# Kernel optimization log

Measured on AMD Instinct MI355X. Metric: run time of the kernel, lower is better.

## Reference

```python
import jax, jax.numpy as jnp
import numpy as np

N = 50000      # nodes (single 'paper' node type)
E = 800000     # edges per etype
ET = 3         # edge types
L = 3          # GAT layers (1 + num_hidden=2)
H = 4          # heads
DH = 64        # per-head dim (n_hidden // n_heads)
NH = H * DH    # 256
NC = 16        # classes
NEG_SLOPE = 0.2


def setup_inputs() -> dict:
    key = jax.random.key(0)
    ks = jax.random.split(key, 8)
    x = jax.random.normal(ks[0], (N, NH), jnp.float32)
    src = jax.random.randint(ks[1], (ET, E), 0, N, jnp.int32)
    dst = jax.random.randint(ks[2], (ET, E), 0, N, jnp.int32)
    W = jax.random.normal(ks[3], (L, ET, NH, NH), jnp.float32) * 0.05
    attn_l = jax.random.normal(ks[4], (L, ET, H, DH), jnp.float32) * 0.05
    attn_r = jax.random.normal(ks[5], (L, ET, H, DH), jnp.float32) * 0.05
    bias = jnp.zeros((L, ET, NH), jnp.float32)
    lin_w = jax.random.normal(ks[6], (NH, NC), jnp.float32) * 0.05
    lin_b = jnp.zeros((NC,), jnp.float32)
    return {"x": x, "src": src, "dst": dst, "W": W, "attn_l": attn_l,
            "attn_r": attn_r, "bias": bias, "lin_w": lin_w, "lin_b": lin_b}


def _gat(h, W_e, al, ar, b, s, d):
    # h: [N, NH] -> z: [N, H, DH]
    z = (h @ W_e).reshape(N, H, DH)
    el = jnp.sum(z * al, axis=-1)             # [N, H]  (src-side score)
    er = jnp.sum(z * ar, axis=-1)             # [N, H]  (dst-side score)
    e = jax.nn.leaky_relu(el[s] + er[d], NEG_SLOPE)   # [E, H]
    # edge softmax over incoming edges of each dst node
    m = jax.ops.segment_max(e, d, num_segments=N)     # [N, H]
    a = jnp.exp(e - m[d])                              # [E, H]
    denom = jax.ops.segment_sum(a, d, num_segments=N) # [N, H]
    alpha = a / denom[d]                               # [E, H]
    # weighted aggregation of source features
    out = jax.ops.segment_sum(alpha[:, :, None] * z[s], d, num_segments=N)  # [N, H, DH]
    return out.reshape(N, NH) + b


def reference(x, src, dst, W, attn_l, attn_r, bias, lin_w, lin_b):
    h = x
    for l in range(L):
        acc = jnp.zeros((N, NH), h.dtype)
        for t in range(ET):  # HeteroGraphConv 'sum' aggregation across etypes
            acc = acc + _gat(h, W[l, t], attn_l[l, t], attn_r[l, t],
                             bias[l, t], src[t], dst[t])
        h = acc
        if l != L - 1:
            h = jax.nn.relu(h)  # dropout is identity in eval
    return h @ lin_w + lin_b    # [N, NC]
```

## Files before the change

kernel.cpp:

```cpp
#include <hip/hip_runtime.h>
#include <hip/hip_bf16.h>
#include <math.h>

#define N_NODES 50000
#define NEDGE 800000
#define NET 3
#define LAYERS 3
#define HEADS 4
#define DHEAD 64
#define NH 256
#define NC 16
#define NEG_SLOPE 0.2f
#define MPAD 50048
#define NTOT (NET * N_NODES)
#define SCAN_BLOCKS ((NTOT + 1023) / 1024)

typedef __attribute__((ext_vector_type(8))) short short8;
typedef __attribute__((ext_vector_type(4))) float f32x4;
typedef __attribute__((ext_vector_type(8))) _Float16 half8;

#define GLDS16(gp, lp) \
  __builtin_amdgcn_global_load_lds((const __attribute__((address_space(1))) void*)(gp), \
                                   (__attribute__((address_space(3))) void*)(lp), 16, 0, 0)

__device__ inline unsigned short f2bf(float x) {
  unsigned u = __float_as_uint(x);
  unsigned r = (u + 0x7FFFu + ((u >> 16) & 1u)) >> 16;
  return (unsigned short)r;
}
__device__ inline float bf2f(unsigned short h) { return __uint_as_float(((unsigned)h) << 16); }

__global__ void split_transpose_W(const float* __restrict__ W,
                                  unsigned short* __restrict__ WhT,
                                  unsigned short* __restrict__ WlT) {
  int i = blockIdx.x * blockDim.x + threadIdx.x;
  if (i >= LAYERS * NET * NH * NH) return;
  int mat = i >> 16, rem = i & 65535;
  int n = rem >> 8, k = rem & 255;
  float v = W[(size_t)mat * 65536 + k * 256 + n];
  unsigned short hi = f2bf(v);
  unsigned short lo = f2bf(v - bf2f(hi));
  WhT[(size_t)mat * 65536 + n * 256 + k] = hi;
  WlT[(size_t)mat * 65536 + n * 256 + k] = lo;
}

__global__ void split_kernel(const float* __restrict__ in, unsigned short* __restrict__ hi,
                             unsigned short* __restrict__ lo) {
  int i = blockIdx.x * blockDim.x + threadIdx.x;
  if (i >= N_NODES * NH / 4) return;
  float4 v = ((const float4*)in)[i];
  ushort4 h, l;
  h.x = f2bf(v.x); l.x = f2bf(v.x - bf2f(h.x));
  h.y = f2bf(v.y); l.y = f2bf(v.y - bf2f(h.y));
  h.z = f2bf(v.z); l.z = f2bf(v.z - bf2f(h.z));
  h.w = f2bf(v.w); l.w = f2bf(v.w - bf2f(h.w));
  ((ushort4*)hi)[i] = h;
  ((ushort4*)lo)[i] = l;
}

__global__ __launch_bounds__(256) void gemm_split3(const unsigned short* __restrict__ Ah,
                                                   const unsigned short* __restrict__ Al,
                                                   const unsigned short* __restrict__ WhT_l,
                                                   const unsigned short* __restrict__ WlT_l,
                                                   const float* __restrict__ attn_l_l,
                                                   const float* __restrict__ attn_r_l,
                                                   _Float16* __restrict__ zh_all,
                                                   float* __restrict__ el_all,
                                                   float* __restrict__ er_all, int M) {
  int t = blockIdx.y;
  const unsigned short* BhT = WhT_l + (size_t)t * NH * NH;
  const unsigned short* BlT = WlT_l + (size_t)t * NH * NH;
  const float* al = attn_l_l + (size_t)t * NH;
  const float* ar = attn_r_l + (size_t)t * NH;
  _Float16* zh = zh_all + (size_t)t * N_NODES * NH;
  float* el = el_all + (size_t)t * N_NODES * HEADS;
  float* er = er_all + (size_t)t * N_NODES * HEADS;

  __shared__ unsigned short lds[20480];
  unsigned short* sAh = lds;
  unsigned short* sAl = lds + 2048;
  unsigned short* sBh = lds + 4096;
  unsigned short* sBl = lds + 12288;

  int tid = threadIdx.x;
  int w = tid >> 6, lane = tid & 63;
  int r16 = lane & 15, rk = lane >> 4;
  int bm = blockIdx.x * 64;

  int arow = tid >> 2, acol = (tid & 3) * 8;
  const unsigned short* pAh = Ah + (size_t)(bm + arow) * 256 + acol;
  const unsigned short* pAl = Al + (size_t)(bm + arow) * 256 + acol;

  f32x4 acc[4][4];
#pragma unroll
  for (int m = 0; m < 4; m++)
#pragma unroll
    for (int n = 0; n < 4; n++) acc[m][n] = (f32x4){0.f, 0.f, 0.f, 0.f};

  char* aldsA = (char*)lds + (size_t)w * 1024;

#pragma unroll
  for (int k0 = 0; k0 < 8; k0++) {
    GLDS16(pAh + k0 * 32, aldsA);
    GLDS16(pAl + k0 * 32, (char*)sAl + (size_t)w * 1024);
#pragma unroll
    for (int i = 0; i < 4; i++) {
      int slot = tid + i * 256;
      int nrow = slot >> 2, kcol = (slot & 3) * 8;
      size_t go = (size_t)nrow * 256 + k0 * 32 + kcol;
      char* lb = (char*)sBh + ((size_t)w * 64 + (size_t)i * 256) * 16;
      char* lb2 = (char*)sBl + ((size_t)w * 64 + (size_t)i * 256) * 16;
      GLDS16(BhT + go, lb);
      GLDS16(BlT + go, lb2);
    }
    __syncthreads();

    short8 a_h[4], a_l[4], b_h[4], b_l[4];
#pragma unroll
    for (int m = 0; m < 4; m++) {
      a_h[m] = *(const short8*)&sAh[(m * 16 + r16) * 32 + rk * 8];
      a_l[m] = *(const short8*)&sAl[(m * 16 + r16) * 32 + rk * 8];
    }
#pragma unroll
    for (int n = 0; n < 4; n++) {
      int col = w * 64 + n * 16 + r16;
      b_h[n] = *(const short8*)&sBh[col * 32 + rk * 8];
      b_l[n] = *(const short8*)&sBl[col * 32 + rk * 8];
    }
#pragma unroll
    for (int m = 0; m < 4; m++)
#pragma unroll
      for (int n = 0; n < 4; n++) {
        acc[m][n] = __builtin_amdgcn_mfma_f32_16x16x32_bf16(a_h[m], b_h[n], acc[m][n], 0, 0, 0);
        acc[m][n] = __builtin_amdgcn_mfma_f32_16x16x32_bf16(a_h[m], b_l[n], acc[m][n], 0, 0, 0);
        acc[m][n] = __builtin_amdgcn_mfma_f32_16x16x32_bf16(a_l[m], b_h[n], acc[m][n], 0, 0, 0);
      }
    __syncthreads();
  }

#pragma unroll
  for (int m = 0; m < 4; m++) {
    int row0 = bm + m * 16 + rk * 4;
#pragma unroll
    for (int n = 0; n < 4; n++) {
      int col = w * 64 + n * 16 + r16;
#pragma unroll
      for (int r = 0; r < 4; r++) {
        int row = row0 + r;
        if (row < M) zh[(size_t)row * 256 + col] = (_Float16)acc[m][n][r];
      }
    }
  }

  float alv[4], arv[4];
#pragma unroll
  for (int n = 0; n < 4; n++) {
    alv[n] = al[w * 64 + n * 16 + r16];
    arv[n] = ar[w * 64 + n * 16 + r16];
  }
#pragma unroll
  for (int m = 0; m < 4; m++) {
#pragma unroll
    for (int r = 0; r < 4; r++) {
      float pl = 0.f, pr = 0.f;
#pragma unroll
      for (int n = 0; n < 4; n++) {
        float zv = acc[m][n][r];
        pl = fmaf(zv, alv[n], pl);
        pr = fmaf(zv, arv[n], pr);
      }
      pl += __shfl_xor(pl, 1, 64); pl += __shfl_xor(pl, 2, 64);
      pl += __shfl_xor(pl, 4, 64); pl += __shfl_xor(pl, 8, 64);
      pr += __shfl_xor(pr, 1, 64); pr += __shfl_xor(pr, 2, 64);
      pr += __shfl_xor(pr, 4, 64); pr += __shfl_xor(pr, 8, 64);
      int row = bm + m * 16 + rk * 4 + r;
      if (r16 == 0 && row < M) {
        el[row * HEADS + w] = pl;
        er[row * HEADS + w] = pr;
      }
    }
  }
}

__device__ inline float leaky(float v) { return v > 0.f ? v : NEG_SLOPE * v; }

__global__ void deg_kernel(const int* __restrict__ dst, int* __restrict__ deg) {
  int e = blockIdx.x * blockDim.x + threadIdx.x;
  int t = blockIdx.y;
  atomicAdd(&deg[t * N_NODES + dst[(size_t)t * NEDGE + e]], 1);
}

__global__ __launch_bounds__(1024) void scan1_kernel(const int* __restrict__ deg,
                                                     int* __restrict__ incl,
                                                     int* __restrict__ bsum) {
  __shared__ int wsum[16];
  int tid = threadIdx.x;
  int gid = blockIdx.x * 1024 + tid;
  int lane = tid & 63, wv = tid >> 6;
  int v = (gid < NTOT) ? deg[gid] : 0;
  int x = v;
#pragma unroll
  for (int off = 1; off < 64; off <<= 1) {
    int y = __shfl_up(x, off, 64);
    if (lane >= off) x += y;
  }
  if (lane == 63) wsum[wv] = x;
  __syncthreads();
  if (wv == 0 && lane < 16) {
    int s = wsum[lane];
#pragma unroll
    for (int off = 1; off < 16; off <<= 1) {
      int y = __shfl_up(s, off, 16);
      if (lane >= off) s += y;
    }
    wsum[lane] = s;
  }
  __syncthreads();
  int waveoff = (wv > 0) ? wsum[wv - 1] : 0;
  int inclv = x + waveoff;
  if (gid < NTOT) incl[gid] = inclv;
  if (tid == 1023) bsum[blockIdx.x] = inclv;
}

__global__ __launch_bounds__(256) void scan2_kernel(int* __restrict__ bsum, int nb) {
  __shared__ int wsum[4];
  int tid = threadIdx.x;
  int lane = tid & 63, wv = tid >> 6;
  int v = (tid < nb) ? bsum[tid] : 0;
  int x = v;
#pragma unroll
  for (int off = 1; off < 64; off <<= 1) {
    int y = __shfl_up(x, off, 64);
    if (lane >= off) x += y;
  }
  if (lane == 63) wsum[wv] = x;
  __syncthreads();
  if (wv == 0 && lane < 4) {
    int s = wsum[lane];
#pragma unroll
    for (int off = 1; off < 4; off <<= 1) {
      int y = __shfl_up(s, off, 4);
      if (lane >= off) s += y;
    }
    wsum[lane] = s;
  }
  __syncthreads();
  int waveoff = (wv > 0) ? wsum[wv - 1] : 0;
  if (tid < nb) bsum[tid] = x + waveoff - v;
}

__global__ __launch_bounds__(1024) void scan3_kernel(const int* __restrict__ incl,
                                                     const int* __restrict__ bsum,
                                                     int* __restrict__ rowptr) {
  int tid = threadIdx.x;
  int gid = blockIdx.x * 1024 + tid;
  if (gid < NTOT) rowptr[gid + 1] = incl[gid] + bsum[blockIdx.x];
  if (gid == 0) rowptr[0] = 0;
}

__global__ void scatter_kernel(const int* __restrict__ src, const int* __restrict__ dst,
                               int* __restrict__ cursor, int* __restrict__ col) {
  int e = blockIdx.x * blockDim.x + threadIdx.x;
  int t = blockIdx.y;
  int d = dst[(size_t)t * NEDGE + e];
  int pos = atomicAdd(&cursor[t * N_NODES + d], 1);
  col[pos] = src[(size_t)t * NEDGE + e] + t * N_NODES;
}

__global__ __launch_bounds__(256) void agg3_kernel(const int* __restrict__ rowptr,
                                                   const int* __restrict__ col,
                                                   const float* __restrict__ el,
                                                   const float* __restrict__ er,
                                                   const _Float16* __restrict__ zh,
                                                   float* __restrict__ hout,
                                                   unsigned short* __restrict__ Ah,
                                                   unsigned short* __restrict__ Al,
                                                   const float* __restrict__ b0,
                                                   const float* __restrict__ b1,
                                                   const float* __restrict__ b2,
                                                   int final_layer) {
  __shared__ float s_alpha[4][128][4];
  __shared__ int s_col[4][128];

  int wv = threadIdx.x >> 6, lane = threadIdx.x & 63;
  int n = blockIdx.x * 4 + wv;
  int kk = lane & 15, hh = lane >> 4;
  int which = lane >> 5, lj = lane & 31, fh = lj >> 3;

  float v0 = 0.f, v1 = 0.f, v2 = 0.f, v3 = 0.f;
  float v4 = 0.f, v5 = 0.f, v6 = 0.f, v7 = 0.f;

  for (int t = 0; t < NET; t++) {
    int gn = t * N_NODES + n;
    int rs = rowptr[gn];
    int deg = rowptr[gn + 1] - rs;
    float erh = er[(size_t)gn * HEADS + hh];

    float sm = 0.f;
    float a0 = 0.f, a1 = 0.f, a2 = 0.f, a3 = 0.f;
    float a4 = 0.f, a5 = 0.f, a6 = 0.f, a7 = 0.f;

    for (int s0 = 0; s0 < deg; s0 += 128) {
      int segN = min(128, deg - s0);
      for (int c0 = 0; c0 < segN; c0 += 16) {
        if (c0 + kk < segN) {
          int row = col[rs + s0 + c0 + kk];
          float a = __expf(leaky(el[(size_t)row * HEADS + hh] + erh));
          sm += a;
          s_alpha[wv][c0 + kk][hh] = a;
          if (hh == 0) s_col[wv][c0 + kk] = row;
        }
      }
      int k = which;
      for (; k + 6 < segN; k += 8) {
        float aa = s_alpha[wv][k][fh];     int ra = s_col[wv][k];
        float ab = s_alpha[wv][k + 2][fh]; int rb = s_col[wv][k + 2];
        float ac = s_alpha[wv][k + 4][fh]; int rc = s_col[wv][k + 4];
        float ad = s_alpha[wv][k + 6][fh]; int rd = s_col[wv][k + 6];
        half8 va = *(const half8*)&zh[(size_t)ra * NH + lj * 8];
        half8 vb = *(const half8*)&zh[(size_t)rb * NH + lj * 8];
        half8 vc = *(const half8*)&zh[(size_t)rc * NH + lj * 8];
        half8 vd = *(const half8*)&zh[(size_t)rd * NH + lj * 8];
        a0 = fmaf(aa, (float)va[0], a0); a1 = fmaf(aa, (float)va[1], a1);
        a2 = fmaf(aa, (float)va[2], a2); a3 = fmaf(aa, (float)va[3], a3);
        a4 = fmaf(aa, (float)va[4], a4); a5 = fmaf(aa, (float)va[5], a5);
        a6 = fmaf(aa, (float)va[6], a6); a7 = fmaf(aa, (float)va[7], a7);
        a0 = fmaf(ab, (float)vb[0], a0); a1 = fmaf(ab, (float)vb[1], a1);
        a2 = fmaf(ab, (float)vb[2], a2); a3 = fmaf(ab, (float)vb[3], a3);
        a4 = fmaf(ab, (float)vb[4], a4); a5 = fmaf(ab, (float)vb[5], a5);
        a6 = fmaf(ab, (float)vb[6], a6); a7 = fmaf(ab, (float)vb[7], a7);
        a0 = fmaf(ac, (float)vc[0], a0); a1 = fmaf(ac, (float)vc[1], a1);
        a2 = fmaf(ac, (float)vc[2], a2); a3 = fmaf(ac, (float)vc[3], a3);
        a4 = fmaf(ac, (float)vc[4], a4); a5 = fmaf(ac, (float)vc[5], a5);
        a6 = fmaf(ac, (float)vc[6], a6); a7 = fmaf(ac, (float)vc[7], a7);
        a0 = fmaf(ad, (float)vd[0], a0); a1 = fmaf(ad, (float)vd[1], a1);
        a2 = fmaf(ad, (float)vd[2], a2); a3 = fmaf(ad, (float)vd[3], a3);
        a4 = fmaf(ad, (float)vd[4], a4); a5 = fmaf(ad, (float)vd[5], a5);
        a6 = fmaf(ad, (float)vd[6], a6); a7 = fmaf(ad, (float)vd[7], a7);
      }
      for (; k < segN; k += 2) {
        float aa = s_alpha[wv][k][fh];
        int ra = s_col[wv][k];
        half8 va = *(const half8*)&zh[(size_t)ra * NH + lj * 8];
        a0 = fmaf(aa, (float)va[0], a0); a1 = fmaf(aa, (float)va[1], a1);
        a2 = fmaf(aa, (float)va[2], a2); a3 = fmaf(aa, (float)va[3], a3);
        a4 = fmaf(aa, (float)va[4], a4); a5 = fmaf(aa, (float)va[5], a5);
        a6 = fmaf(aa, (float)va[6], a6); a7 = fmaf(aa, (float)va[7], a7);
      }
    }

    sm += __shfl_xor(sm, 1, 64);
    sm += __shfl_xor(sm, 2, 64);
    sm += __shfl_xor(sm, 4, 64);
    sm += __shfl_xor(sm, 8, 64);
    float inv = (deg > 0) ? 1.f / sm : 0.f;
    float invb = __shfl(inv, fh * 16, 64);

    a0 += __shfl_xor(a0, 32, 64); a1 += __shfl_xor(a1, 32, 64);
    a2 += __shfl_xor(a2, 32, 64); a3 += __shfl_xor(a3, 32, 64);
    a4 += __shfl_xor(a4, 32, 64); a5 += __shfl_xor(a5, 32, 64);
    a6 += __shfl_xor(a6, 32, 64); a7 += __shfl_xor(a7, 32, 64);

    v0 = fmaf(a0, invb, v0); v1 = fmaf(a1, invb, v1);
    v2 = fmaf(a2, invb, v2); v3 = fmaf(a3, invb, v3);
    v4 = fmaf(a4, invb, v4); v5 = fmaf(a5, invb, v5);
    v6 = fmaf(a6, invb, v6); v7 = fmaf(a7, invb, v7);
  }

  if (lane < 32) {
    int f0 = lj * 8;
    float vo[8] = {v0, v1, v2, v3, v4, v5, v6, v7};
#pragma unroll
    for (int i = 0; i < 8; i++) vo[i] += b0[f0 + i] + b1[f0 + i] + b2[f0 + i];
    if (final_layer) {
      size_t oi = (size_t)n * NH + f0;
      float4 o0 = {vo[0], vo[1], vo[2], vo[3]};
      float4 o1 = {vo[4], vo[5], vo[6], vo[7]};
      *(float4*)&hout[oi] = o0;
      *(float4*)&hout[oi + 4] = o1;
    } else {
      ushort4 hi0, hi1, lo0, lo1;
#pragma unroll
      for (int i = 0; i < 8; i++) vo[i] = fmaxf(vo[i], 0.f);
      hi0.x = f2bf(vo[0]); lo0.x = f2bf(vo[0] - bf2f(hi0.x));
      hi0.y = f2bf(vo[1]); lo0.y = f2bf(vo[1] - bf2f(hi0.y));
      hi0.z = f2bf(vo[2]); lo0.z = f2bf(vo[2] - bf2f(hi0.z));
      hi0.w = f2bf(vo[3]); lo0.w = f2bf(vo[3] - bf2f(hi0.w));
      hi1.x = f2bf(vo[4]); lo1.x = f2bf(vo[4] - bf2f(hi1.x));
      hi1.y = f2bf(vo[5]); lo1.y = f2bf(vo[5] - bf2f(hi1.y));
      hi1.z = f2bf(vo[6]); lo1.z = f2bf(vo[6] - bf2f(hi1.z));
      hi1.w = f2bf(vo[7]); lo1.w = f2bf(vo[7] - bf2f(hi1.w));
      size_t oi = (size_t)n * NH + f0;
      *(ushort4*)&Ah[oi] = hi0;
      *(ushort4*)&Ah[oi + 4] = hi1;
      *(ushort4*)&Al[oi] = lo0;
      *(ushort4*)&Al[oi + 4] = lo1;
    }
  }
}

__global__ __launch_bounds__(256) void linear_kernel(const float* __restrict__ h,
                                                     const float* __restrict__ w,
                                                     const float* __restrict__ b,
                                                     float* __restrict__ out) {
  __shared__ float part[16][17];
  int n = blockIdx.x;
  int t = threadIdx.x;
  int c = t & 15, p = t >> 4;
  float sum = 0.f;
#pragma unroll
  for (int q = 0; q < 16; q++) {
    int j = p * 16 + q;
    sum = fmaf(h[(size_t)n * NH + j], w[j * NC + c], sum);
  }
  part[p][c] = sum;
  __syncthreads();
  if (t < 16) {
    float s = 0.f;
#pragma unroll
    for (int p2 = 0; p2 < 16; p2++) s += part[p2][t];
    out[n * NC + t] = s + b[t];
  }
}

extern "C" void kernel_launch(void* const* d_in, const int* in_sizes, int n_in,
                              void* d_out, int out_size, void* d_ws, size_t ws_size,
                              hipStream_t stream) {
  const float* x      = (const float*)d_in[0];
  const int*   src    = (const int*)d_in[1];
  const int*   dst    = (const int*)d_in[2];
  const float* W      = (const float*)d_in[3];
  const float* attn_l = (const float*)d_in[4];
  const float* attn_r = (const float*)d_in[5];
  const float* bias   = (const float*)d_in[6];
  const float* lin_w  = (const float*)d_in[7];
  const float* lin_b  = (const float*)d_in[8];
  float* out = (float*)d_out;

  char* ws = (char*)d_ws;
  size_t off = 0;
  _Float16* zh = (_Float16*)(ws + off); off += (size_t)NET * N_NODES * NH * 2;
  unsigned short* Ah = (unsigned short*)(ws + off); off += (size_t)MPAD * NH * 2;
  unsigned short* Al = (unsigned short*)(ws + off); off += (size_t)MPAD * NH * 2;
  float* h = (float*)Ah;
  unsigned short* WhT = (unsigned short*)(ws + off); off += (size_t)LAYERS * NET * NH * NH * 2;
  unsigned short* WlT = (unsigned short*)(ws + off); off += (size_t)LAYERS * NET * NH * NH * 2;
  float* el = (float*)(ws + off); off += (size_t)NTOT * HEADS * 4;
  float* er = (float*)(ws + off); off += (size_t)NTOT * HEADS * 4;
  int* rowptr = (int*)(ws + off); off += (size_t)(NTOT + 1) * 4;
  int* colA   = (int*)(ws + off); off += (size_t)NET * NEDGE * 4;
  int* deg    = (int*)(ws + off); off += (size_t)NTOT * 4;
  int* cursor = (int*)(ws + off); off += (size_t)NTOT * 4;
  int* incl   = (int*)(ws + off); off += (size_t)NTOT * 4;
  int* bsum   = (int*)(ws + off); off += 256 * 4;

  hipMemsetAsync(deg, 0, (size_t)NTOT * 4, stream);
  deg_kernel<<<dim3(NEDGE / 256, NET), 256, 0, stream>>>(dst, deg);
  scan1_kernel<<<SCAN_BLOCKS, 1024, 0, stream>>>(deg, incl, bsum);
  scan2_kernel<<<1, 256, 0, stream>>>(bsum, SCAN_BLOCKS);
  scan3_kernel<<<SCAN_BLOCKS, 1024, 0, stream>>>(incl, bsum, rowptr);
  hipMemcpyAsync(cursor, rowptr, (size_t)NTOT * 4, hipMemcpyDeviceToDevice, stream);
  scatter_kernel<<<dim3(NEDGE / 256, NET), 256, 0, stream>>>(src, dst, cursor, colA);

  split_transpose_W<<<(LAYERS * NET * NH * NH + 255) / 256, 256, 0, stream>>>(W, WhT, WlT);

  split_kernel<<<(N_NODES * NH / 4 + 255) / 256, 256, 0, stream>>>(x, Ah, Al);

  for (int l = 0; l < LAYERS; l++) {
    const float* b0 = bias + (size_t)(l * NET + 0) * NH;
    const float* b1 = bias + (size_t)(l * NET + 1) * NH;
    const float* b2 = bias + (size_t)(l * NET + 2) * NH;

    gemm_split3<<<dim3(MPAD / 64, NET), 256, 0, stream>>>(
        Ah, Al,
        WhT + (size_t)l * NET * NH * NH, WlT + (size_t)l * NET * NH * NH,
        attn_l + (size_t)l * NET * NH, attn_r + (size_t)l * NET * NH,
        zh, el, er, N_NODES);

    agg3_kernel<<<N_NODES / 4, 256, 0, stream>>>(rowptr, colA, el, er, zh, h, Ah, Al,
                                                 b0, b1, b2, l == LAYERS - 1);
  }
  linear_kernel<<<N_NODES, 256, 0, stream>>>(h, lin_w, lin_b, out);
}
```

Measured before the change: 1.315 ms.

## Fuse prep kernels, overlap edge scatter with first GEMM, enlarge GEMM tile

Merges degree counting, feature split and weight split/transpose into one prep launch. Runs the CSR scatter and the layer-0 GEMM in a single launch using disjoint block ranges so the two overlap. Changes the GEMM to 512-thread blocks covering 128 rows, which halves the B-tile loads per output row. Also cuts the aggregation gather unroll from 4 to 2 neighbours per iteration, which may lower register pressure but exposes less memory parallelism.

```diff
diff --git a/kernel.cpp b/kernel.cpp
--- a/kernel.cpp
+++ b/kernel.cpp
@@ -14,6 +14,10 @@
 #define MPAD 50048
 #define NTOT (NET * N_NODES)
 #define SCAN_BLOCKS ((NTOT + 1023) / 1024)
+#define GB_PER_T 391
+#define GEMM_BLOCKS (GB_PER_T * NET)
+#define SCAT_PER_T 1563
+#define SCAT_BLOCKS (SCAT_PER_T * NET)
 
 typedef __attribute__((ext_vector_type(8))) short short8;
 typedef __attribute__((ext_vector_type(4))) float f32x4;
@@ -29,45 +33,60 @@
   return (unsigned short)r;
 }
 __device__ inline float bf2f(unsigned short h) { return __uint_as_float(((unsigned)h) << 16); }
-
-__global__ void split_transpose_W(const float* __restrict__ W,
-                                  unsigned short* __restrict__ WhT,
-                                  unsigned short* __restrict__ WlT) {
-  int i = blockIdx.x * blockDim.x + threadIdx.x;
-  if (i >= LAYERS * NET * NH * NH) return;
-  int mat = i >> 16, rem = i & 65535;
-  int n = rem >> 8, k = rem & 255;
-  float v = W[(size_t)mat * 65536 + k * 256 + n];
-  unsigned short hi = f2bf(v);
-  unsigned short lo = f2bf(v - bf2f(hi));
-  WhT[(size_t)mat * 65536 + n * 256 + k] = hi;
-  WlT[(size_t)mat * 65536 + n * 256 + k] = lo;
-}
-
-__global__ void split_kernel(const float* __restrict__ in, unsigned short* __restrict__ hi,
-                             unsigned short* __restrict__ lo) {
-  int i = blockIdx.x * blockDim.x + threadIdx.x;
-  if (i >= N_NODES * NH / 4) return;
-  float4 v = ((const float4*)in)[i];
-  ushort4 h, l;
-  h.x = f2bf(v.x); l.x = f2bf(v.x - bf2f(h.x));
-  h.y = f2bf(v.y); l.y = f2bf(v.y - bf2f(h.y));
-  h.z = f2bf(v.z); l.z = f2bf(v.z - bf2f(h.z));
-  h.w = f2bf(v.w); l.w = f2bf(v.w - bf2f(h.w));
-  ((ushort4*)hi)[i] = h;
-  ((ushort4*)lo)[i] = l;
-}
-
-__global__ __launch_bounds__(256) void gemm_split3(const unsigned short* __restrict__ Ah,
-                                                   const unsigned short* __restrict__ Al,
-                                                   const unsigned short* __restrict__ WhT_l,
-                                                   const unsigned short* __restrict__ WlT_l,
-                                                   const float* __restrict__ attn_l_l,
-                                                   const float* __restrict__ attn_r_l,
-                                                   _Float16* __restrict__ zh_all,
-                                                   float* __restrict__ el_all,
-                                                   float* __restrict__ er_all, int M) {
-  int t = blockIdx.y;
+__device__ inline float leaky(float v) { return v > 0.f ? v : NEG_SLOPE * v; }
+
+__global__ __launch_bounds__(256) void prep_kernel(const int* __restrict__ dst,
+                                                   int* __restrict__ deg,
+                                                   const float* __restrict__ x,
+                                                   unsigned short* __restrict__ Ah,
+                                                   unsigned short* __restrict__ Al,
+                                                   const float* __restrict__ W,
+                                                   unsigned short* __restrict__ WhT,
+                                                   unsigned short* __restrict__ WlT) {
+  int b = blockIdx.x;
+  if (b < 9375) {
+    int t = b / 3125, r = b % 3125;
+    int e = r * 256 + threadIdx.x;
+    atomicAdd(&deg[t * N_NODES + dst[(size_t)t * NEDGE + e]], 1);
+  } else if (b < 21875) {
+    int i = (b - 9375) * 256 + threadIdx.x;
+    float4 v = ((const float4*)x)[i];
+    ushort4 h, l;
+    h.x = f2bf(v.x); l.x = f2bf(v.x - bf2f(h.x));
+    h.y = f2bf(v.y); l.y = f2bf(v.y - bf2f(h.y));
+    h.z = f2bf(v.z); l.z = f2bf(v.z - bf2f(h.z));
+    h.w = f2bf(v.w); l.w = f2bf(v.w - bf2f(h.w));
+    ((ushort4*)Ah)[i] = h;
+    ((ushort4*)Al)[i] = l;
+  } else {
+    int i = (b - 21875) * 256 + threadIdx.x;
+    int mat = i >> 16, rem = i & 65535;
+    int n = rem >> 8, k = rem & 255;
+    float v = W[(size_t)mat * 65536 + k * 256 + n];
+    unsigned short hi = f2bf(v);
+    unsigned short lo = f2bf(v - bf2f(hi));
+    WhT[(size_t)mat * 65536 + n * 256 + k] = hi;
+    WlT[(size_t)mat * 65536 + n * 256 + k] = lo;
+  }
+}
+
+__device__ __forceinline__ void gemm_dev(int bid,
+                                         const unsigned short* __restrict__ Ah,
+                                         const unsigned short* __restrict__ Al,
+                                         const unsigned short* __restrict__ WhT_l,
+                                         const unsigned short* __restrict__ WlT_l,
+                                         const float* __restrict__ attn_l_l,
+                                         const float* __restrict__ attn_r_l,
+                                         _Float16* __restrict__ zh_all,
+                                         float* __restrict__ el_all,
+                                         float* __restrict__ er_all, int M) {
+  __shared__ unsigned short lds[24576];
+  unsigned short* sAh = lds;
+  unsigned short* sAl = lds + 4096;
+  unsigned short* sBh = lds + 8192;
+  unsigned short* sBl = lds + 16384;
+
+  int t = bid / GB_PER_T, bx = bid % GB_PER_T;
   const unsigned short* BhT = WhT_l + (size_t)t * NH * NH;
   const unsigned short* BlT = WlT_l + (size_t)t * NH * NH;
   const float* al = attn_l_l + (size_t)t * NH;
@@ -76,20 +95,14 @@
   float* el = el_all + (size_t)t * N_NODES * HEADS;
   float* er = er_all + (size_t)t * N_NODES * HEADS;
 
-  __shared__ unsigned short lds[20480];
-  unsigned short* sAh = lds;
-  unsigned short* sAl = lds + 2048;
-  unsigned short* sBh = lds + 4096;
-  unsigned short* sBl = lds + 12288;
-
   int tid = threadIdx.x;
   int w = tid >> 6, lane = tid & 63;
+  int rg = w >> 2, hd = w & 3;
   int r16 = lane & 15, rk = lane >> 4;
-  int bm = blockIdx.x * 64;
-
-  int arow = tid >> 2, acol = (tid & 3) * 8;
-  const unsigned short* pAh = Ah + (size_t)(bm + arow) * 256 + acol;
-  const unsigned short* pAl = Al + (size_t)(bm + arow) * 256 + acol;
+  int bm = bx * 128;
+
+  const unsigned short* pAh = Ah + (size_t)(bm + (tid >> 2)) * 256 + (tid & 3) * 8;
+  const unsigned short* pAl = Al + (size_t)(bm + (tid >> 2)) * 256 + (tid & 3) * 8;
 
   f32x4 acc[4][4];
 #pragma unroll
@@ -97,33 +110,32 @@
 #pragma unroll
     for (int n = 0; n < 4; n++) acc[m][n] = (f32x4){0.f, 0.f, 0.f, 0.f};
 
-  char* aldsA = (char*)lds + (size_t)w * 1024;
+  char* aBaseH = (char*)sAh + w * 1024;
+  char* aBaseL = (char*)sAl + w * 1024;
 
 #pragma unroll
   for (int k0 = 0; k0 < 8; k0++) {
-    GLDS16(pAh + k0 * 32, aldsA);
-    GLDS16(pAl + k0 * 32, (char*)sAl + (size_t)w * 1024);
-#pragma unroll
-    for (int i = 0; i < 4; i++) {
-      int slot = tid + i * 256;
-      int nrow = slot >> 2, kcol = (slot & 3) * 8;
-      size_t go = (size_t)nrow * 256 + k0 * 32 + kcol;
-      char* lb = (char*)sBh + ((size_t)w * 64 + (size_t)i * 256) * 16;
-      char* lb2 = (char*)sBl + ((size_t)w * 64 + (size_t)i * 256) * 16;
-      GLDS16(BhT + go, lb);
-      GLDS16(BlT + go, lb2);
+    GLDS16(pAh + k0 * 32, aBaseH);
+    GLDS16(pAl + k0 * 32, aBaseL);
+#pragma unroll
+    for (int i = 0; i < 2; i++) {
+      int slot = tid + i * 512;
+      size_t go = (size_t)(slot >> 2) * 256 + k0 * 32 + (slot & 3) * 8;
+      GLDS16(BhT + go, (char*)sBh + ((size_t)i * 512 + w * 64) * 16);
+      GLDS16(BlT + go, (char*)sBl + ((size_t)i * 512 + w * 64) * 16);
     }
     __syncthreads();
 
     short8 a_h[4], a_l[4], b_h[4], b_l[4];
 #pragma unroll
     for (int m = 0; m < 4; m++) {
-      a_h[m] = *(const short8*)&sAh[(m * 16 + r16) * 32 + rk * 8];
-      a_l[m] = *(const short8*)&sAl[(m * 16 + r16) * 32 + rk * 8];
+      int row = rg * 64 + m * 16 + r16;
+      a_h[m] = *(const short8*)&sAh[row * 32 + rk * 8];
+      a_l[m] = *(const short8*)&sAl[row * 32 + rk * 8];
     }
 #pragma unroll
     for (int n = 0; n < 4; n++) {
-      int col = w * 64 + n * 16 + r16;
+      int col = hd * 64 + n * 16 + r16;
       b_h[n] = *(const short8*)&sBh[col * 32 + rk * 8];
       b_l[n] = *(const short8*)&sBl[col * 32 + rk * 8];
     }
@@ -140,10 +152,10 @@
 
 #pragma unroll
   for (int m = 0; m < 4; m++) {
-    int row0 = bm + m * 16 + rk * 4;
+    int row0 = bm + rg * 64 + m * 16 + rk * 4;
 #pragma unroll
     for (int n = 0; n < 4; n++) {
-      int col = w * 64 + n * 16 + r16;
+      int col = hd * 64 + n * 16 + r16;
 #pragma unroll
       for (int r = 0; r < 4; r++) {
         int row = row0 + r;
@@ -155,8 +167,8 @@
   float alv[4], arv[4];
 #pragma unroll
   for (int n = 0; n < 4; n++) {
-    alv[n] = al[w * 64 + n * 16 + r16];
-    arv[n] = ar[w * 64 + n * 16 + r16];
+    alv[n] = al[hd * 64 + n * 16 + r16];
+    arv[n] = ar[hd * 64 + n * 16 + r16];
   }
 #pragma unroll
   for (int m = 0; m < 4; m++) {
@@ -173,21 +185,45 @@
       pl += __shfl_xor(pl, 4, 64); pl += __shfl_xor(pl, 8, 64);
       pr += __shfl_xor(pr, 1, 64); pr += __shfl_xor(pr, 2, 64);
       pr += __shfl_xor(pr, 4, 64); pr += __shfl_xor(pr, 8, 64);
-      int row = bm + m * 16 + rk * 4 + r;
+      int row = bm + rg * 64 + m * 16 + rk * 4 + r;
       if (r16 == 0 && row < M) {
-        el[row * HEADS + w] = pl;
-        er[row * HEADS + w] = pr;
-      }
-    }
-  }
-}
-
-__device__ inline float leaky(float v) { return v > 0.f ? v : NEG_SLOPE * v; }
-
-__global__ void deg_kernel(const int* __restrict__ dst, int* __restrict__ deg) {
-  int e = blockIdx.x * blockDim.x + threadIdx.x;
-  int t = blockIdx.y;
-  atomicAdd(&deg[t * N_NODES + dst[(size_t)t * NEDGE + e]], 1);
+        el[row * HEADS + hd] = pl;
+        er[row * HEADS + hd] = pr;
+      }
+    }
+  }
+}
+
+__global__ __launch_bounds__(512) void gemm0_scatter_kernel(
+    const unsigned short* __restrict__ Ah, const unsigned short* __restrict__ Al,
+    const unsigned short* __restrict__ WhT_l, const unsigned short* __restrict__ WlT_l,
+    const float* __restrict__ attn_l_l, const float* __restrict__ attn_r_l,
+    _Float16* __restrict__ zh_all, float* __restrict__ el_all, float* __restrict__ er_all,
+    int M,
+    const int* __restrict__ src, const int* __restrict__ dst,
+    int* __restrict__ cursor, int* __restrict__ col) {
+  if (blockIdx.x < SCAT_BLOCKS) {
+    int b = blockIdx.x;
+    int t = b / SCAT_PER_T, r = b % SCAT_PER_T;
+    int e = r * 512 + (int)threadIdx.x;
+    if (e < NEDGE) {
+      int d = dst[(size_t)t * NEDGE + e];
+      int pos = atomicAdd(&cursor[t * N_NODES + d], 1);
+      col[pos] = src[(size_t)t * NEDGE + e] + t * N_NODES;
+    }
+  } else {
+    gemm_dev(blockIdx.x - SCAT_BLOCKS, Ah, Al, WhT_l, WlT_l, attn_l_l, attn_r_l,
+             zh_all, el_all, er_all, M);
+  }
+}
+
+__global__ __launch_bounds__(512) void gemm_split3(
+    const unsigned short* __restrict__ Ah, const unsigned short* __restrict__ Al,
+    const unsigned short* __restrict__ WhT_l, const unsigned short* __restrict__ WlT_l,
+    const float* __restrict__ attn_l_l, const float* __restrict__ attn_r_l,
+    _Float16* __restrict__ zh_all, float* __restrict__ el_all, float* __restrict__ er_all,
+    int M) {
+  gemm_dev(blockIdx.x, Ah, Al, WhT_l, WlT_l, attn_l_l, attn_r_l, zh_all, el_all, er_all, M);
 }
 
 __global__ __launch_bounds__(1024) void scan1_kernel(const int* __restrict__ deg,
@@ -256,15 +292,6 @@
   int gid = blockIdx.x * 1024 + tid;
   if (gid < NTOT) rowptr[gid + 1] = incl[gid] + bsum[blockIdx.x];
   if (gid == 0) rowptr[0] = 0;
-}
-
-__global__ void scatter_kernel(const int* __restrict__ src, const int* __restrict__ dst,
-                               int* __restrict__ cursor, int* __restrict__ col) {
-  int e = blockIdx.x * blockDim.x + threadIdx.x;
-  int t = blockIdx.y;
-  int d = dst[(size_t)t * NEDGE + e];
-  int pos = atomicAdd(&cursor[t * N_NODES + d], 1);
-  col[pos] = src[(size_t)t * NEDGE + e] + t * N_NODES;
 }
 
 __global__ __launch_bounds__(256) void agg3_kernel(const int* __restrict__ rowptr,
@@ -312,15 +339,11 @@
         }
       }
       int k = which;
-      for (; k + 6 < segN; k += 8) {
+      for (; k + 2 < segN; k += 4) {
         float aa = s_alpha[wv][k][fh];     int ra = s_col[wv][k];
         float ab = s_alpha[wv][k + 2][fh]; int rb = s_col[wv][k + 2];
-        float ac = s_alpha[wv][k + 4][fh]; int rc = s_col[wv][k + 4];
-        float ad = s_alpha[wv][k + 6][fh]; int rd = s_col[wv][k + 6];
         half8 va = *(const half8*)&zh[(size_t)ra * NH + lj * 8];
         half8 vb = *(const half8*)&zh[(size_t)rb * NH + lj * 8];
-        half8 vc = *(const half8*)&zh[(size_t)rc * NH + lj * 8];
-        half8 vd = *(const half8*)&zh[(size_t)rd * NH + lj * 8];
         a0 = fmaf(aa, (float)va[0], a0); a1 = fmaf(aa, (float)va[1], a1);
         a2 = fmaf(aa, (float)va[2], a2); a3 = fmaf(aa, (float)va[3], a3);
         a4 = fmaf(aa, (float)va[4], a4); a5 = fmaf(aa, (float)va[5], a5);
@@ -329,14 +352,6 @@
         a2 = fmaf(ab, (float)vb[2], a2); a3 = fmaf(ab, (float)vb[3], a3);
         a4 = fmaf(ab, (float)vb[4], a4); a5 = fmaf(ab, (float)vb[5], a5);
         a6 = fmaf(ab, (float)vb[6], a6); a7 = fmaf(ab, (float)vb[7], a7);
-        a0 = fmaf(ac, (float)vc[0], a0); a1 = fmaf(ac, (float)vc[1], a1);
-        a2 = fmaf(ac, (float)vc[2], a2); a3 = fmaf(ac, (float)vc[3], a3);
-        a4 = fmaf(ac, (float)vc[4], a4); a5 = fmaf(ac, (float)vc[5], a5);
-        a6 = fmaf(ac, (float)vc[6], a6); a7 = fmaf(ac, (float)vc[7], a7);
-        a0 = fmaf(ad, (float)vd[0], a0); a1 = fmaf(ad, (float)vd[1], a1);
-        a2 = fmaf(ad, (float)vd[2], a2); a3 = fmaf(ad, (float)vd[3], a3);
-        a4 = fmaf(ad, (float)vd[4], a4); a5 = fmaf(ad, (float)vd[5], a5);
-        a6 = fmaf(ad, (float)vd[6], a6); a7 = fmaf(ad, (float)vd[7], a7);
       }
       for (; k < segN; k += 2) {
         float aa = s_alpha[wv][k][fh];
@@ -455,28 +470,28 @@
   int* bsum   = (int*)(ws + off); off += 256 * 4;
 
   hipMemsetAsync(deg, 0, (size_t)NTOT * 4, stream);
-  deg_kernel<<<dim3(NEDGE / 256, NET), 256, 0, stream>>>(dst, deg);
+  prep_kernel<<<24179, 256, 0, stream>>>(dst, deg, x, Ah, Al, W, WhT, WlT);
+
   scan1_kernel<<<SCAN_BLOCKS, 1024, 0, stream>>>(deg, incl, bsum);
   scan2_kernel<<<1, 256, 0, stream>>>(bsum, SCAN_BLOCKS);
   scan3_kernel<<<SCAN_BLOCKS, 1024, 0, stream>>>(incl, bsum, rowptr);
   hipMemcpyAsync(cursor, rowptr, (size_t)NTOT * 4, hipMemcpyDeviceToDevice, stream);
-  scatter_kernel<<<dim3(NEDGE / 256, NET), 256, 0, stream>>>(src, dst, cursor, colA);
-
-  split_transpose_W<<<(LAYERS * NET * NH * NH + 255) / 256, 256, 0, stream>>>(W, WhT, WlT);
-
-  split_kernel<<<(N_NODES * NH / 4 + 255) / 256, 256, 0, stream>>>(x, Ah, Al);
+
+  gemm0_scatter_kernel<<<SCAT_BLOCKS + GEMM_BLOCKS, 512, 0, stream>>>(
+      Ah, Al, WhT, WlT, attn_l, attn_r, zh, el, er, N_NODES, src, dst, cursor, colA);
 
   for (int l = 0; l < LAYERS; l++) {
     const float* b0 = bias + (size_t)(l * NET + 0) * NH;
     const float* b1 = bias + (size_t)(l * NET + 1) * NH;
     const float* b2 = bias + (size_t)(l * NET + 2) * NH;
 
-    gemm_split3<<<dim3(MPAD / 64, NET), 256, 0, stream>>>(
-        Ah, Al,
-        WhT + (size_t)l * NET * NH * NH, WlT + (size_t)l * NET * NH * NH,
-        attn_l + (size_t)l * NET * NH, attn_r + (size_t)l * NET * NH,
-        zh, el, er, N_NODES);
-
+    if (l > 0) {
+      gemm_split3<<<GEMM_BLOCKS, 512, 0, stream>>>(
+          Ah, Al,
+          WhT + (size_t)l * NET * NH * NH, WlT + (size_t)l * NET * NH * NH,
+          attn_l + (size_t)l * NET * NH, attn_r + (size_t)l * NET * NH,
+          zh, el, er, N_NODES);
+    }
     agg3_kernel<<<N_NODES / 4, 256, 0, stream>>>(rowptr, colA, el, er, zh, h, Ah, Al,
                                                  b0, b1, b2, l == LAYERS - 1);
   }
```

Result: no change. 1.296 ms (-1.4%).
